# Kernel tuning notes

Measured on AMD Instinct MI355X. Metric: run time of the kernel, lower is better.

The kernel has to match this reference:

```python
import jax, jax.numpy as jnp
import numpy as np

B, N = 8, 2048
ZD, SD, MLP, DEPTH = 512, 64, 2048, 4


def setup_inputs() -> dict:
    key = jax.random.key(0)
    ks = jax.random.split(key, 8)
    g = lambda k, shape: jax.random.normal(k, shape, jnp.float32) * 0.02
    return {
        "z": jax.random.normal(ks[0], (B, N, ZD), jnp.float32),
        "spatial_embedding": jax.random.normal(ks[1], (B, N, SD), jnp.float32) * 0.5,
        "ln_z_scale": jnp.ones((DEPTH, ZD), jnp.float32),
        "ln_z_bias": jnp.zeros((DEPTH, ZD), jnp.float32),
        "ln_s_scale": jnp.ones((DEPTH, ZD), jnp.float32),
        "ln_s_bias": jnp.zeros((DEPTH, ZD), jnp.float32),
        "Wz1": g(ks[2], (DEPTH, ZD, MLP)), "bz1": jnp.zeros((DEPTH, MLP), jnp.float32),
        "Wz2": g(ks[3], (DEPTH, MLP, ZD)), "bz2": jnp.zeros((DEPTH, ZD), jnp.float32),
        "Ws1": g(ks[4], (DEPTH, ZD, MLP)), "bs1": jnp.zeros((DEPTH, MLP), jnp.float32),
        "Ws2": g(ks[5], (DEPTH, MLP, SD)), "bs2": jnp.zeros((DEPTH, SD), jnp.float32),
    }


def _layernorm(x, scale, bias, eps=1e-5):
    m = jnp.mean(x, axis=-1, keepdims=True)
    v = jnp.var(x, axis=-1, keepdims=True)  # biased var, matches torch LayerNorm
    return (x - m) * jax.lax.rsqrt(v + eps) * scale + bias


def _spatial_attn(e, z):
    # sim = exp(-||e_i - e_j||^2), row-normalized == softmax(-d2) over j.
    # Use |a|^2 + |b|^2 - 2ab expansion to avoid the [B,N,N,D] broadcast tensor.
    sq = jnp.sum(e * e, axis=-1)  # [B,N]
    d2 = sq[:, :, None] + sq[:, None, :] - 2.0 * jnp.einsum('bid,bjd->bij', e, e)
    d2 = jnp.maximum(d2, 0.0)
    attn = jax.nn.softmax(-d2, axis=-1)  # [B,N,N]
    return jnp.einsum('bij,bjd->bid', attn, z)


def _ff(x, W1, b1, W2, b2):
    h = jax.nn.gelu(x @ W1 + b1, approximate=False)  # torch nn.GELU() is exact erf
    return h @ W2 + b2


def reference(z, spatial_embedding, ln_z_scale, ln_z_bias, ln_s_scale, ln_s_bias,
              Wz1, bz1, Wz2, bz2, Ws1, bs1, Ws2, bs2):
    s = spatial_embedding
    for i in range(DEPTH):
        z = _spatial_attn(s, z)
        z = _ff(_layernorm(z, ln_z_scale[i], ln_z_bias[i]), Wz1[i], bz1[i], Wz2[i], bz2[i]) + z
        s = _ff(_layernorm(z, ln_s_scale[i], ln_s_bias[i]), Ws1[i], bs1[i], Ws2[i], bs2[i]) + s
    return (z, s)
```

## Files before the change

kernel.cpp:

```cpp
#include <hip/hip_runtime.h>
#include <stdint.h>

#define DEPTH 4
#define BATCH 8
#define NN 2048
#define ZDIM 512
#define SDIM 64
#define MLPD 2048
#define ROWS (BATCH*NN)

typedef __bf16 bf16x8_t __attribute__((ext_vector_type(8)));
typedef float f32x4_t __attribute__((ext_vector_type(4)));
typedef unsigned short us;

#define AS1 __attribute__((address_space(1)))
#define AS3 __attribute__((address_space(3)))

__device__ __forceinline__ void gload16(const void* g, void* l) {
  __builtin_amdgcn_global_load_lds((const AS1 void*)g, (AS3 void*)l, 16, 0, 0);
}

__device__ __forceinline__ unsigned short f2bf(float f) {
  union { float f; unsigned u; } v; v.f = f;
  unsigned u = v.u;
  unsigned r = (u + 0x7fffu + ((u >> 16) & 1u)) >> 16;
  return (unsigned short)r;
}
__device__ __forceinline__ float bf2f(unsigned short h) {
  union { unsigned u; float f; } v; v.u = ((unsigned)h) << 16;
  return v.f;
}

__device__ __forceinline__ float gelu_fast(float x) {
  float ax = fabsf(x) * 0.70710678118654752440f;
  float t = __builtin_amdgcn_rcpf(1.0f + 0.3275911f * ax);
  float p = t * (0.254829592f + t * (-0.284496736f + t * (1.421413741f +
            t * (-1.453152027f + t * 1.061405429f))));
  float er = 1.0f - p * __expf(-ax * ax);
  float s = (x >= 0.f) ? er : -er;
  return 0.5f * x * (1.0f + s);
}

#define LGKM0() do { asm volatile("s_waitcnt lgkmcnt(0)" ::: "memory"); \
                     __builtin_amdgcn_sched_barrier(0); } while (0)

__global__ __launch_bounds__(256) void conv_e_kernel(const float* __restrict__ s,
    unsigned short* __restrict__ ebf, float* __restrict__ sq) {
  int lane = threadIdx.x & 63;
  int row = blockIdx.x * 4 + (threadIdx.x >> 6);
  float x = s[(long)row * SDIM + lane];
  unsigned short v = f2bf(x);
  ebf[(long)row * SDIM + lane] = v;
  float xb = bf2f(v);
  float ss = xb * xb;
  #pragma unroll
  for (int off = 32; off > 0; off >>= 1) ss += __shfl_xor(ss, off);
  if (lane == 0) sq[row] = ss;
}

__global__ __launch_bounds__(256) void tconv_kernel(const float* __restrict__ in,
    unsigned short* __restrict__ out, int R, int C, long sIn, long sOut) {
  __shared__ float tile[32][33];
  int b = blockIdx.z;
  int c0 = blockIdx.x * 32, r0 = blockIdx.y * 32;
  int tx = threadIdx.x, ty = threadIdx.y;
  const float* ib = in + (long)b * sIn;
  unsigned short* ob = out + (long)b * sOut;
  #pragma unroll
  for (int i = 0; i < 32; i += 8)
    tile[ty + i][tx] = ib[(long)(r0 + ty + i) * C + c0 + tx];
  __syncthreads();
  #pragma unroll
  for (int i = 0; i < 32; i += 8)
    ob[(long)(c0 + ty + i) * R + r0 + tx] = f2bf(tile[tx][ty + i]);
}

__global__ __launch_bounds__(256) void ln_kernel(const float* __restrict__ x,
    const float* __restrict__ scale, const float* __restrict__ bias,
    unsigned short* __restrict__ y) {
  int lane = threadIdx.x & 63;
  long row = (long)blockIdx.x * 4 + (threadIdx.x >> 6);
  const float* xr = x + row * ZDIM + lane * 8;
  float4 v0 = *(const float4*)xr;
  float4 v1 = *(const float4*)(xr + 4);
  float xv[8] = {v0.x, v0.y, v0.z, v0.w, v1.x, v1.y, v1.z, v1.w};
  float s1 = 0.f, s2 = 0.f;
  #pragma unroll
  for (int k = 0; k < 8; ++k) { s1 += xv[k]; s2 += xv[k] * xv[k]; }
  #pragma unroll
  for (int off = 32; off > 0; off >>= 1) {
    s1 += __shfl_xor(s1, off);
    s2 += __shfl_xor(s2, off);
  }
  float mean = s1 * (1.0f / ZDIM);
  float var = s2 * (1.0f / ZDIM) - mean * mean;
  float rstd = rsqrtf(var + 1e-5f);
  const float* sc = scale + lane * 8;
  const float* bi = bias + lane * 8;
  alignas(16) unsigned short o[8];
  #pragma unroll
  for (int k = 0; k < 8; ++k)
    o[k] = f2bf((xv[k] - mean) * rstd * sc[k] + bi[k]);
  *(uint4*)(y + row * ZDIM + lane * 8) = *(const uint4*)o;
}

__global__ __launch_bounds__(256) void attn_w_kernel(const unsigned short* __restrict__ ebf,
    const float* __restrict__ sq, unsigned short* __restrict__ wout,
    float* __restrict__ RS) {
  __shared__ unsigned short Ei[4096];
  __shared__ unsigned short Ej[8192];
  __shared__ unsigned short Wt[8192];
  int tid = threadIdx.x, lane = tid & 63, wid = tid >> 6;
  int lr = lane & 15, hi = lane >> 4;
  int q = blockIdx.y;
  int b = blockIdx.z;
  int i0 = blockIdx.x * 64;
  const unsigned short* eb = ebf + (long)b * NN * SDIM;

  int rl = tid >> 3;
  int scs = ((tid & 7) ^ (rl & 7)) * 8;
  int dstc = (tid & 192) * 8;

  #pragma unroll
  for (int it = 0; it < 2; ++it)
    gload16(eb + (long)(i0 + it * 32 + rl) * SDIM + scs, &Ei[it * 2048 + dstc]);
  #pragma unroll
  for (int it = 0; it < 4; ++it)
    gload16(eb + (long)(q * 512 + it * 32 + rl) * SDIM + scs, &Ej[it * 2048 + dstc]);
  __syncthreads();

  bf16x8_t afrag[2];
  int ka = lr & 7;
  #pragma unroll
  for (int s = 0; s < 2; ++s)
    afrag[s] = *(const bf16x8_t*)&Ei[(wid * 16 + lr) * 64 + (((s * 4 + hi) ^ ka) * 8)];
  int rloc = wid * 16 + (hi << 2);
  float sqi[4];
  #pragma unroll
  for (int r = 0; r < 4; ++r) sqi[r] = sq[b * NN + i0 + rloc + r];
  float rs[4] = {0.f, 0.f, 0.f, 0.f};
  us* stripe = &Wt[wid * 2048];

  for (int jj = 0; jj < 4; ++jj) {
    int j0 = q * 512 + jj * 128;
    if (jj > 0) {
      __syncthreads();
      #pragma unroll
      for (int it = 0; it < 4; ++it)
        gload16(eb + (long)(j0 + it * 32 + rl) * SDIM + scs, &Ej[it * 2048 + dstc]);
      __syncthreads();
    }
    #pragma unroll
    for (int n = 0; n < 8; ++n) {
      f32x4_t g = {0.f, 0.f, 0.f, 0.f};
      #pragma unroll
      for (int s = 0; s < 2; ++s) {
        int rb = n * 16 + lr;
        bf16x8_t bfr = *(const bf16x8_t*)&Ej[rb * 64 + (((s * 4 + hi) ^ (rb & 7)) * 8)];
        g = __builtin_amdgcn_mfma_f32_16x16x32_bf16(afrag[s], bfr, g, 0, 0, 0);
      }
      float sqj = sq[b * NN + j0 + n * 16 + lr];
      #pragma unroll
      for (int r = 0; r < 4; ++r) {
        float d2 = sqi[r] + sqj - 2.0f * g[r];
        d2 = fmaxf(d2, 0.0f);
        float w = __expf(-d2);
        unsigned short wb = f2bf(w);
        rs[r] += bf2f(wb);
        int srow = (hi << 2) + r;
        stripe[srow * 128 + ((n ^ (srow & 3)) * 16) + lr] = wb;
      }
    }
    LGKM0();
    #pragma unroll
    for (int it = 0; it < 4; ++it) {
      int seg = it * 64 + lane;
      int row = seg >> 4, c8 = seg & 15;
      int c8s = c8 ^ ((row & 3) << 1);
      uint4 v = *(const uint4*)&stripe[row * 128 + c8s * 8];
      long gi = i0 + wid * 16 + row;
      *(uint4*)&wout[(long)b * NN * NN + gi * NN + j0 + c8 * 8] = v;
    }
  }
  #pragma unroll
  for (int off = 1; off < 16; off <<= 1) {
    #pragma unroll
    for (int r = 0; r < 4; ++r) rs[r] += __shfl_xor(rs[r], off);
  }
  if (lr == 0) {
    #pragma unroll
    for (int r = 0; r < 4; ++r)
      RS[(long)q * ROWS + b * NN + i0 + rloc + r] = rs[r];
  }
}

template <int EPI>
__global__ __launch_bounds__(256, 4) void gemm3b(
    const unsigned short* __restrict__ A, const unsigned short* __restrict__ BT,
    void* __restrict__ Cout, const float* __restrict__ bias,
    const float* __restrict__ resid, const float* __restrict__ RS,
    int Nmat, int K, long sA, long sB, long sC, long sR) {
  __shared__ unsigned short As[64 * 64];
  __shared__ unsigned short Bs[128 * 64];
  int tid = threadIdx.x, lane = tid & 63;
  int lr = lane & 15, hi = lane >> 4;
  int wid = tid >> 6, wr = wid >> 1, wc = wid & 1;
  int bb = blockIdx.z;

  int gx = gridDim.x;
  int wg = blockIdx.y * gx + blockIdx.x;
  int nwg = gx * gridDim.y;
  if ((nwg & 7) == 0) wg = (wg & 7) * (nwg >> 3) + (wg >> 3);
  int bj = wg % gx, bi = wg / gx;
  int row0 = bi * 64, col0 = bj * 128;

  const unsigned short* Ab = A + (long)bb * sA;
  const unsigned short* Bb = BT + (long)bb * sB;

  int rl = tid >> 3;
  int scs = ((tid & 7) ^ (rl & 7)) * 8;
  const unsigned short* pA[2];
  const unsigned short* pB[4];
  #pragma unroll
  for (int it = 0; it < 2; ++it)
    pA[it] = Ab + (long)(row0 + it * 32 + rl) * K + scs;
  #pragma unroll
  for (int it = 0; it < 4; ++it) {
    int rb = col0 + it * 32 + rl;
    if (rb > Nmat - 1) rb = Nmat - 1;
    pB[it] = Bb + (long)rb * K + scs;
  }
  int dstc = (tid & 192) * 8;

  int offA[2][2], offB[4][2];
  #pragma unroll
  for (int m = 0; m < 2; ++m)
    #pragma unroll
    for (int s = 0; s < 2; ++s) {
      int ra = wr * 32 + m * 16 + lr;
      offA[m][s] = ra * 64 + (((s * 4 + hi) ^ (ra & 7)) * 8);
    }
  #pragma unroll
  for (int n = 0; n < 4; ++n)
    #pragma unroll
    for (int s = 0; s < 2; ++s) {
      int rb = wc * 64 + n * 16 + lr;
      offB[n][s] = rb * 64 + (((s * 4 + hi) ^ (rb & 7)) * 8);
    }

  auto stage = [&]() {
    #pragma unroll
    for (int it = 0; it < 2; ++it) { gload16(pA[it], &As[it * 2048 + dstc]); pA[it] += 64; }
    #pragma unroll
    for (int it = 0; it < 4; ++it) { gload16(pB[it], &Bs[it * 2048 + dstc]); pB[it] += 64; }
  };

  const f32x4_t fzero = {0.f, 0.f, 0.f, 0.f};
  f32x4_t acc[2][4];
  #pragma unroll
  for (int m = 0; m < 2; ++m)
    #pragma unroll
    for (int n = 0; n < 4; ++n) acc[m][n] = fzero;

  int nk = K >> 6;
  stage();

  for (int t = 0; t < nk; ++t) {
    __syncthreads();
    bf16x8_t a0s0 = *(const bf16x8_t*)&As[offA[0][0]];
    bf16x8_t a1s0 = *(const bf16x8_t*)&As[offA[1][0]];
    bf16x8_t a0s1 = *(const bf16x8_t*)&As[offA[0][1]];
    bf16x8_t a1s1 = *(const bf16x8_t*)&As[offA[1][1]];
    bf16x8_t b0s0 = *(const bf16x8_t*)&Bs[offB[0][0]];
    bf16x8_t b1s0 = *(const bf16x8_t*)&Bs[offB[1][0]];
    bf16x8_t b2s0 = *(const bf16x8_t*)&Bs[offB[2][0]];
    bf16x8_t b3s0 = *(const bf16x8_t*)&Bs[offB[3][0]];
    bf16x8_t b0s1 = *(const bf16x8_t*)&Bs[offB[0][1]];
    bf16x8_t b1s1 = *(const bf16x8_t*)&Bs[offB[1][1]];
    bf16x8_t b2s1 = *(const bf16x8_t*)&Bs[offB[2][1]];
    bf16x8_t b3s1 = *(const bf16x8_t*)&Bs[offB[3][1]];
    __syncthreads();
    if (t + 1 < nk) stage();
    acc[0][0] = __builtin_amdgcn_mfma_f32_16x16x32_bf16(a0s0, b0s0, acc[0][0], 0, 0, 0);
    acc[1][0] = __builtin_amdgcn_mfma_f32_16x16x32_bf16(a1s0, b0s0, acc[1][0], 0, 0, 0);
    acc[0][1] = __builtin_amdgcn_mfma_f32_16x16x32_bf16(a0s0, b1s0, acc[0][1], 0, 0, 0);
    acc[1][1] = __builtin_amdgcn_mfma_f32_16x16x32_bf16(a1s0, b1s0, acc[1][1], 0, 0, 0);
    acc[0][2] = __builtin_amdgcn_mfma_f32_16x16x32_bf16(a0s0, b2s0, acc[0][2], 0, 0, 0);
    acc[1][2] = __builtin_amdgcn_mfma_f32_16x16x32_bf16(a1s0, b2s0, acc[1][2], 0, 0, 0);
    acc[0][3] = __builtin_amdgcn_mfma_f32_16x16x32_bf16(a0s0, b3s0, acc[0][3], 0, 0, 0);
    acc[1][3] = __builtin_amdgcn_mfma_f32_16x16x32_bf16(a1s0, b3s0, acc[1][3], 0, 0, 0);
    acc[0][0] = __builtin_amdgcn_mfma_f32_16x16x32_bf16(a0s1, b0s1, acc[0][0], 0, 0, 0);
    acc[1][0] = __builtin_amdgcn_mfma_f32_16x16x32_bf16(a1s1, b0s1, acc[1][0], 0, 0, 0);
    acc[0][1] = __builtin_amdgcn_mfma_f32_16x16x32_bf16(a0s1, b1s1, acc[0][1], 0, 0, 0);
    acc[1][1] = __builtin_amdgcn_mfma_f32_16x16x32_bf16(a1s1, b1s1, acc[1][1], 0, 0, 0);
    acc[0][2] = __builtin_amdgcn_mfma_f32_16x16x32_bf16(a0s1, b2s1, acc[0][2], 0, 0, 0);
    acc[1][2] = __builtin_amdgcn_mfma_f32_16x16x32_bf16(a1s1, b2s1, acc[1][2], 0, 0, 0);
    acc[0][3] = __builtin_amdgcn_mfma_f32_16x16x32_bf16(a0s1, b3s1, acc[0][3], 0, 0, 0);
    acc[1][3] = __builtin_amdgcn_mfma_f32_16x16x32_bf16(a1s1, b3s1, acc[1][3], 0, 0, 0);
  }

  int rbase = row0 + wr * 32 + hi * 4;
  int cbase = col0 + wc * 64 + lr;
  if (EPI == 1) {
    float bv[4];
    #pragma unroll
    for (int n = 0; n < 4; ++n) bv[n] = bias[cbase + n * 16];
    us* stripe = &Bs[wid * 2048];
    #pragma unroll
    for (int m = 0; m < 2; ++m) {
      #pragma unroll
      for (int r = 0; r < 4; ++r) {
        int sr = m * 16 + hi * 4 + r;
        #pragma unroll
        for (int n = 0; n < 4; ++n)
          stripe[sr * 64 + ((n ^ (sr & 3)) * 16) + lr] =
              f2bf(gelu_fast(acc[m][n][r] + bv[n]));
      }
    }
    LGKM0();
    unsigned short* Cb = (unsigned short*)Cout;
    #pragma unroll
    for (int it = 0; it < 4; ++it) {
      int seg = it * 64 + lane;
      int sr = seg >> 3, c8 = seg & 7;
      int c8s = c8 ^ ((sr & 3) << 1);
      uint4 v = *(const uint4*)&stripe[sr * 64 + c8s * 8];
      long row = row0 + wr * 32 + sr;
      *(uint4*)&Cb[row * Nmat + col0 + wc * 64 + c8 * 8] = v;
    }
  } else {
    #pragma unroll
    for (int m = 0; m < 2; ++m) {
      #pragma unroll
      for (int r = 0; r < 4; ++r) {
        int row = rbase + m * 16 + r;
        float ir = 0.f;
        if (EPI == 0) {
          long idx = (long)bb * sR + row;
          float den = RS[idx] + RS[ROWS + idx] + RS[2L * ROWS + idx] + RS[3L * ROWS + idx];
          ir = 1.0f / den;
        }
        #pragma unroll
        for (int n = 0; n < 4; ++n) {
          int col = cbase + n * 16;
          if (col >= Nmat) continue;
          float v = acc[m][n][r];
          long cidx = (long)bb * sC + (long)row * Nmat + col;
          if (EPI == 0) {
            ((float*)Cout)[cidx] = v * ir;
          } else {
            ((float*)Cout)[cidx] = v + bias[col] + resid[(long)bb * sR + (long)row * Nmat + col];
          }
        }
      }
    }
  }
}

extern "C" void kernel_launch(void* const* d_in, const int* in_sizes, int n_in,
                              void* d_out, int out_size, void* d_ws, size_t ws_size,
                              hipStream_t stream) {
  (void)in_sizes; (void)n_in; (void)out_size; (void)ws_size;
  const float* in_z   = (const float*)d_in[0];
  const float* in_s   = (const float*)d_in[1];
  const float* lnz_sc = (const float*)d_in[2];
  const float* lnz_bi = (const float*)d_in[3];
  const float* lns_sc = (const float*)d_in[4];
  const float* lns_bi = (const float*)d_in[5];
  const float* Wz1 = (const float*)d_in[6];
  const float* bz1 = (const float*)d_in[7];
  const float* Wz2 = (const float*)d_in[8];
  const float* bz2 = (const float*)d_in[9];
  const float* Ws1 = (const float*)d_in[10];
  const float* bs1 = (const float*)d_in[11];
  const float* Ws2 = (const float*)d_in[12];
  const float* bs2 = (const float*)d_in[13];
  float* out_z = (float*)d_out;
  float* out_s = out_z + (long)ROWS * ZDIM;

  char* ws = (char*)d_ws;
  size_t off = 0;
  auto alloc = [&](size_t bytes) { void* p = ws + off; off += (bytes + 255) & ~(size_t)255; return p; };
  unsigned short* WH   = (unsigned short*)alloc((size_t)BATCH * NN * NN * 2);
  unsigned short* ZT   = (unsigned short*)alloc((size_t)BATCH * ZDIM * NN * 2);
  unsigned short* XLN  = (unsigned short*)alloc((size_t)ROWS * ZDIM * 2);
  unsigned short* EBF  = (unsigned short*)alloc((size_t)ROWS * SDIM * 2);
  float* ZATT = (float*)alloc((size_t)ROWS * ZDIM * 4);
  float* ZBUF = (float*)alloc((size_t)ROWS * ZDIM * 4);
  float* SBUF = (float*)alloc((size_t)ROWS * SDIM * 4);
  float* SQ   = (float*)alloc((size_t)ROWS * 4);
  float* RS   = (float*)alloc((size_t)4 * ROWS * 4);
  unsigned short* W1Z = (unsigned short*)alloc((size_t)DEPTH * MLPD * ZDIM * 2);
  unsigned short* W2Z = (unsigned short*)alloc((size_t)DEPTH * ZDIM * MLPD * 2);
  unsigned short* W1S = (unsigned short*)alloc((size_t)DEPTH * MLPD * ZDIM * 2);
  unsigned short* W2S = (unsigned short*)alloc((size_t)DEPTH * SDIM * MLPD * 2);

  tconv_kernel<<<dim3(MLPD / 32, ZDIM / 32, DEPTH), dim3(32, 8), 0, stream>>>(
      Wz1, W1Z, ZDIM, MLPD, (long)ZDIM * MLPD, (long)MLPD * ZDIM);
  tconv_kernel<<<dim3(ZDIM / 32, MLPD / 32, DEPTH), dim3(32, 8), 0, stream>>>(
      Wz2, W2Z, MLPD, ZDIM, (long)MLPD * ZDIM, (long)ZDIM * MLPD);
  tconv_kernel<<<dim3(MLPD / 32, ZDIM / 32, DEPTH), dim3(32, 8), 0, stream>>>(
      Ws1, W1S, ZDIM, MLPD, (long)ZDIM * MLPD, (long)MLPD * ZDIM);
  tconv_kernel<<<dim3(SDIM / 32, MLPD / 32, DEPTH), dim3(32, 8), 0, stream>>>(
      Ws2, W2S, MLPD, SDIM, (long)MLPD * SDIM, (long)SDIM * MLPD);

  for (int L = 0; L < DEPTH; ++L) {
    const float* z_in = (L == 0) ? in_z : ZBUF;
    const float* s_in = (L == 0) ? in_s : SBUF;
    float* z_out = (L == DEPTH - 1) ? out_z : ZBUF;
    float* s_out = (L == DEPTH - 1) ? out_s : SBUF;

    conv_e_kernel<<<ROWS / 4, 256, 0, stream>>>(s_in, EBF, SQ);
    tconv_kernel<<<dim3(ZDIM / 32, NN / 32, BATCH), dim3(32, 8), 0, stream>>>(
        z_in, ZT, NN, ZDIM, (long)NN * ZDIM, (long)ZDIM * NN);
    attn_w_kernel<<<dim3(NN / 64, 4, BATCH), 256, 0, stream>>>(EBF, SQ, WH, RS);
    gemm3b<0><<<dim3(ZDIM / 128, NN / 64, BATCH), 256, 0, stream>>>(
        WH, ZT, ZATT, nullptr, nullptr, RS,
        ZDIM, NN, (long)NN * NN, (long)ZDIM * NN, (long)NN * ZDIM, NN);
    ln_kernel<<<ROWS / 4, 256, 0, stream>>>(ZATT, lnz_sc + L * ZDIM, lnz_bi + L * ZDIM, XLN);
    gemm3b<1><<<dim3(MLPD / 128, ROWS / 64, 1), 256, 0, stream>>>(
        XLN, W1Z + (long)L * MLPD * ZDIM, WH, bz1 + L * MLPD, nullptr, nullptr,
        MLPD, ZDIM, 0, 0, 0, 0);
    gemm3b<2><<<dim3(ZDIM / 128, ROWS / 64, 1), 256, 0, stream>>>(
        WH, W2Z + (long)L * ZDIM * MLPD, z_out, bz2 + L * ZDIM, ZATT, nullptr,
        ZDIM, MLPD, 0, 0, 0, 0);
    ln_kernel<<<ROWS / 4, 256, 0, stream>>>(z_out, lns_sc + L * ZDIM, lns_bi + L * ZDIM, XLN);
    gemm3b<1><<<dim3(MLPD / 128, ROWS / 64, 1), 256, 0, stream>>>(
        XLN, W1S + (long)L * MLPD * ZDIM, WH, bs1 + L * MLPD, nullptr, nullptr,
        MLPD, ZDIM, 0, 0, 0, 0);
    gemm3b<2><<<dim3(1, ROWS / 64, 1), 256, 0, stream>>>(
        WH, W2S + (long)L * SDIM * MLPD, s_out, bs2 + L * SDIM, s_in, nullptr,
        SDIM, MLPD, 0, 0, 0, 0);
  }
}
```

Measured before the change: 1.125 ms.

## Fuse attention weight computation with PV GEMM in a flash-style kernel

```diff
diff --git a/kernel.cpp b/kernel.cpp
--- a/kernel.cpp
+++ b/kernel.cpp
@@ -43,6 +43,7 @@
 
 #define LGKM0() do { asm volatile("s_waitcnt lgkmcnt(0)" ::: "memory"); \
                      __builtin_amdgcn_sched_barrier(0); } while (0)
+#define MF(A_, B_, C_) __builtin_amdgcn_mfma_f32_16x16x32_bf16(A_, B_, C_, 0, 0, 0)
 
 __global__ __launch_bounds__(256) void conv_e_kernel(const float* __restrict__ s,
     unsigned short* __restrict__ ebf, float* __restrict__ sq) {
@@ -104,93 +105,143 @@
   *(uint4*)(y + row * ZDIM + lane * 8) = *(const uint4*)o;
 }
 
-__global__ __launch_bounds__(256) void attn_w_kernel(const unsigned short* __restrict__ ebf,
-    const float* __restrict__ sq, unsigned short* __restrict__ wout,
-    float* __restrict__ RS) {
-  __shared__ unsigned short Ei[4096];
-  __shared__ unsigned short Ej[8192];
-  __shared__ unsigned short Wt[8192];
+__global__ __launch_bounds__(256, 2) void attn_pv_kernel(
+    const unsigned short* __restrict__ ebf, const float* __restrict__ sq,
+    const unsigned short* __restrict__ ZTg, float* __restrict__ Oout) {
+  __shared__ unsigned short Ei[2048];
+  __shared__ unsigned short Ej[2][8192];
+  __shared__ unsigned short Pl[2][4096];
+  __shared__ float RSs[4][32];
   int tid = threadIdx.x, lane = tid & 63, wid = tid >> 6;
   int lr = lane & 15, hi = lane >> 4;
-  int q = blockIdx.y;
   int b = blockIdx.z;
-  int i0 = blockIdx.x * 64;
+  int i0 = blockIdx.x * 32;
   const unsigned short* eb = ebf + (long)b * NN * SDIM;
+  const unsigned short* zb = ZTg + (long)b * ZDIM * NN;
 
   int rl = tid >> 3;
   int scs = ((tid & 7) ^ (rl & 7)) * 8;
   int dstc = (tid & 192) * 8;
 
-  #pragma unroll
-  for (int it = 0; it < 2; ++it)
-    gload16(eb + (long)(i0 + it * 32 + rl) * SDIM + scs, &Ei[it * 2048 + dstc]);
+  gload16(eb + (long)(i0 + rl) * SDIM + scs, &Ei[dstc]);
   #pragma unroll
   for (int it = 0; it < 4; ++it)
-    gload16(eb + (long)(q * 512 + it * 32 + rl) * SDIM + scs, &Ej[it * 2048 + dstc]);
+    gload16(eb + (long)(it * 32 + rl) * SDIM + scs, &Ej[0][it * 2048 + dstc]);
+
+  float sqi[2][4];
+  #pragma unroll
+  for (int m = 0; m < 2; ++m)
+    #pragma unroll
+    for (int r = 0; r < 4; ++r)
+      sqi[m][r] = sq[b * NN + i0 + m * 16 + hi * 4 + r];
+
+  const unsigned short* bp[8];
+  #pragma unroll
+  for (int n = 0; n < 8; ++n)
+    bp[n] = zb + (long)(wid * 128 + n * 16 + lr) * NN + hi * 8;
+
+  f32x4_t acc[2][8];
+  #pragma unroll
+  for (int m = 0; m < 2; ++m)
+    #pragma unroll
+    for (int n = 0; n < 8; ++n) acc[m][n] = (f32x4_t){0.f, 0.f, 0.f, 0.f};
+  float rsum[2][4] = {{0.f, 0.f, 0.f, 0.f}, {0.f, 0.f, 0.f, 0.f}};
+
   __syncthreads();
 
-  bf16x8_t afrag[2];
   int ka = lr & 7;
-  #pragma unroll
-  for (int s = 0; s < 2; ++s)
-    afrag[s] = *(const bf16x8_t*)&Ei[(wid * 16 + lr) * 64 + (((s * 4 + hi) ^ ka) * 8)];
-  int rloc = wid * 16 + (hi << 2);
-  float sqi[4];
-  #pragma unroll
-  for (int r = 0; r < 4; ++r) sqi[r] = sq[b * NN + i0 + rloc + r];
-  float rs[4] = {0.f, 0.f, 0.f, 0.f};
-  us* stripe = &Wt[wid * 2048];
-
-  for (int jj = 0; jj < 4; ++jj) {
-    int j0 = q * 512 + jj * 128;
-    if (jj > 0) {
-      __syncthreads();
+  for (int jt = 0; jt < NN / 128; ++jt) {
+    int buf = jt & 1;
+    int j0 = jt * 128;
+
+    f32x4_t sacc[2][2];
+    #pragma unroll
+    for (int m = 0; m < 2; ++m)
+      #pragma unroll
+      for (int n = 0; n < 2; ++n) sacc[m][n] = (f32x4_t){0.f, 0.f, 0.f, 0.f};
+    #pragma unroll
+    for (int k2 = 0; k2 < 2; ++k2) {
+      int kc = ((k2 * 4 + hi) ^ ka) * 8;
+      bf16x8_t af0 = *(const bf16x8_t*)&Ei[lr * 64 + kc];
+      bf16x8_t af1 = *(const bf16x8_t*)&Ei[(16 + lr) * 64 + kc];
+      bf16x8_t bf0 = *(const bf16x8_t*)&Ej[buf][(wid * 32 + lr) * 64 + kc];
+      bf16x8_t bf1 = *(const bf16x8_t*)&Ej[buf][(wid * 32 + 16 + lr) * 64 + kc];
+      sacc[0][0] = MF(af0, bf0, sacc[0][0]);
+      sacc[1][0] = MF(af1, bf0, sacc[1][0]);
+      sacc[0][1] = MF(af0, bf1, sacc[0][1]);
+      sacc[1][1] = MF(af1, bf1, sacc[1][1]);
+    }
+    float sqj0 = sq[b * NN + j0 + wid * 32 + lr];
+    float sqj1 = sq[b * NN + j0 + wid * 32 + 16 + lr];
+    #pragma unroll
+    for (int m = 0; m < 2; ++m) {
+      #pragma unroll
+      for (int n = 0; n < 2; ++n) {
+        float sqjn = n ? sqj1 : sqj0;
+        #pragma unroll
+        for (int r = 0; r < 4; ++r) {
+          int row = m * 16 + hi * 4 + r;
+          float d2 = fmaxf(sqi[m][r] + sqjn - 2.0f * sacc[m][n][r], 0.0f);
+          unsigned short wb = f2bf(__expf(-d2));
+          rsum[m][r] += bf2f(wb);
+          int c8 = wid * 4 + n * 2 + (lr >> 3);
+          Pl[buf][row * 128 + ((c8 ^ (row & 7)) * 8) + (lr & 7)] = wb;
+        }
+      }
+    }
+    __syncthreads();
+
+    if (jt + 1 < NN / 128) {
       #pragma unroll
       for (int it = 0; it < 4; ++it)
-        gload16(eb + (long)(j0 + it * 32 + rl) * SDIM + scs, &Ej[it * 2048 + dstc]);
-      __syncthreads();
-    }
-    #pragma unroll
-    for (int n = 0; n < 8; ++n) {
-      f32x4_t g = {0.f, 0.f, 0.f, 0.f};
-      #pragma unroll
-      for (int s = 0; s < 2; ++s) {
-        int rb = n * 16 + lr;
-        bf16x8_t bfr = *(const bf16x8_t*)&Ej[rb * 64 + (((s * 4 + hi) ^ (rb & 7)) * 8)];
-        g = __builtin_amdgcn_mfma_f32_16x16x32_bf16(afrag[s], bfr, g, 0, 0, 0);
+        gload16(eb + (long)((jt + 1) * 128 + it * 32 + rl) * SDIM + scs,
+                &Ej[buf ^ 1][it * 2048 + dstc]);
+    }
+
+    bf16x8_t bv[2][8];
+    #pragma unroll
+    for (int n = 0; n < 8; ++n) bv[0][n] = *(const bf16x8_t*)(bp[n] + j0);
+    #pragma unroll
+    for (int kf = 0; kf < 4; ++kf) {
+      int cb = kf & 1;
+      if (kf < 3) {
+        #pragma unroll
+        for (int n = 0; n < 8; ++n)
+          bv[cb ^ 1][n] = *(const bf16x8_t*)(bp[n] + j0 + (kf + 1) * 32);
       }
-      float sqj = sq[b * NN + j0 + n * 16 + lr];
-      #pragma unroll
-      for (int r = 0; r < 4; ++r) {
-        float d2 = sqi[r] + sqj - 2.0f * g[r];
-        d2 = fmaxf(d2, 0.0f);
-        float w = __expf(-d2);
-        unsigned short wb = f2bf(w);
-        rs[r] += bf2f(wb);
-        int srow = (hi << 2) + r;
-        stripe[srow * 128 + ((n ^ (srow & 3)) * 16) + lr] = wb;
+      int pc = ((kf * 4 + hi) ^ ka) * 8;
+      bf16x8_t pa0 = *(const bf16x8_t*)&Pl[buf][lr * 128 + pc];
+      bf16x8_t pa1 = *(const bf16x8_t*)&Pl[buf][(16 + lr) * 128 + pc];
+      #pragma unroll
+      for (int n = 0; n < 8; ++n) {
+        acc[0][n] = MF(pa0, bv[cb][n], acc[0][n]);
+        acc[1][n] = MF(pa1, bv[cb][n], acc[1][n]);
       }
     }
-    LGKM0();
-    #pragma unroll
-    for (int it = 0; it < 4; ++it) {
-      int seg = it * 64 + lane;
-      int row = seg >> 4, c8 = seg & 15;
-      int c8s = c8 ^ ((row & 3) << 1);
-      uint4 v = *(const uint4*)&stripe[row * 128 + c8s * 8];
-      long gi = i0 + wid * 16 + row;
-      *(uint4*)&wout[(long)b * NN * NN + gi * NN + j0 + c8 * 8] = v;
-    }
-  }
-  #pragma unroll
-  for (int off = 1; off < 16; off <<= 1) {
-    #pragma unroll
-    for (int r = 0; r < 4; ++r) rs[r] += __shfl_xor(rs[r], off);
-  }
-  if (lr == 0) {
-    #pragma unroll
-    for (int r = 0; r < 4; ++r)
-      RS[(long)q * ROWS + b * NN + i0 + rloc + r] = rs[r];
+    __syncthreads();
+  }
+
+  #pragma unroll
+  for (int m = 0; m < 2; ++m)
+    #pragma unroll
+    for (int r = 0; r < 4; ++r) {
+      float v = rsum[m][r];
+      v += __shfl_xor(v, 1); v += __shfl_xor(v, 2);
+      v += __shfl_xor(v, 4); v += __shfl_xor(v, 8);
+      if (lr == 0) RSs[wid][m * 16 + hi * 4 + r] = v;
+    }
+  __syncthreads();
+  float* ob = Oout + ((long)b * NN + i0) * ZDIM + wid * 128;
+  #pragma unroll
+  for (int m = 0; m < 2; ++m) {
+    #pragma unroll
+    for (int r = 0; r < 4; ++r) {
+      int row = m * 16 + hi * 4 + r;
+      float inv = 1.0f / (RSs[0][row] + RSs[1][row] + RSs[2][row] + RSs[3][row]);
+      #pragma unroll
+      for (int n = 0; n < 8; ++n)
+        ob[(long)row * ZDIM + n * 16 + lr] = acc[m][n][r] * inv;
+    }
   }
 }
 
@@ -198,14 +249,13 @@
 __global__ __launch_bounds__(256, 4) void gemm3b(
     const unsigned short* __restrict__ A, const unsigned short* __restrict__ BT,
     void* __restrict__ Cout, const float* __restrict__ bias,
-    const float* __restrict__ resid, const float* __restrict__ RS,
-    int Nmat, int K, long sA, long sB, long sC, long sR) {
+    const float* __restrict__ resid,
+    int Nmat, int K, long sC, long sR) {
   __shared__ unsigned short As[64 * 64];
   __shared__ unsigned short Bs[128 * 64];
   int tid = threadIdx.x, lane = tid & 63;
   int lr = lane & 15, hi = lane >> 4;
   int wid = tid >> 6, wr = wid >> 1, wc = wid & 1;
-  int bb = blockIdx.z;
 
   int gx = gridDim.x;
   int wg = blockIdx.y * gx + blockIdx.x;
@@ -214,21 +264,18 @@
   int bj = wg % gx, bi = wg / gx;
   int row0 = bi * 64, col0 = bj * 128;
 
-  const unsigned short* Ab = A + (long)bb * sA;
-  const unsigned short* Bb = BT + (long)bb * sB;
-
   int rl = tid >> 3;
   int scs = ((tid & 7) ^ (rl & 7)) * 8;
   const unsigned short* pA[2];
   const unsigned short* pB[4];
   #pragma unroll
   for (int it = 0; it < 2; ++it)
-    pA[it] = Ab + (long)(row0 + it * 32 + rl) * K + scs;
+    pA[it] = A + (long)(row0 + it * 32 + rl) * K + scs;
   #pragma unroll
   for (int it = 0; it < 4; ++it) {
     int rb = col0 + it * 32 + rl;
     if (rb > Nmat - 1) rb = Nmat - 1;
-    pB[it] = Bb + (long)rb * K + scs;
+    pB[it] = BT + (long)rb * K + scs;
   }
   int dstc = (tid & 192) * 8;
 
@@ -255,12 +302,11 @@
     for (int it = 0; it < 4; ++it) { gload16(pB[it], &Bs[it * 2048 + dstc]); pB[it] += 64; }
   };
 
-  const f32x4_t fzero = {0.f, 0.f, 0.f, 0.f};
   f32x4_t acc[2][4];
   #pragma unroll
   for (int m = 0; m < 2; ++m)
     #pragma unroll
-    for (int n = 0; n < 4; ++n) acc[m][n] = fzero;
+    for (int n = 0; n < 4; ++n) acc[m][n] = (f32x4_t){0.f, 0.f, 0.f, 0.f};
 
   int nk = K >> 6;
   stage();
@@ -281,22 +327,22 @@
     bf16x8_t b3s1 = *(const bf16x8_t*)&Bs[offB[3][1]];
     __syncthreads();
     if (t + 1 < nk) stage();
-    acc[0][0] = __builtin_amdgcn_mfma_f32_16x16x32_bf16(a0s0, b0s0, acc[0][0], 0, 0, 0);
-    acc[1][0] = __builtin_amdgcn_mfma_f32_16x16x32_bf16(a1s0, b0s0, acc[1][0], 0, 0, 0);
-    acc[0][1] = __builtin_amdgcn_mfma_f32_16x16x32_bf16(a0s0, b1s0, acc[0][1], 0, 0, 0);
-    acc[1][1] = __builtin_amdgcn_mfma_f32_16x16x32_bf16(a1s0, b1s0, acc[1][1], 0, 0, 0);
-    acc[0][2] = __builtin_amdgcn_mfma_f32_16x16x32_bf16(a0s0, b2s0, acc[0][2], 0, 0, 0);
-    acc[1][2] = __builtin_amdgcn_mfma_f32_16x16x32_bf16(a1s0, b2s0, acc[1][2], 0, 0, 0);
-    acc[0][3] = __builtin_amdgcn_mfma_f32_16x16x32_bf16(a0s0, b3s0, acc[0][3], 0, 0, 0);
-    acc[1][3] = __builtin_amdgcn_mfma_f32_16x16x32_bf16(a1s0, b3s0, acc[1][3], 0, 0, 0);
-    acc[0][0] = __builtin_amdgcn_mfma_f32_16x16x32_bf16(a0s1, b0s1, acc[0][0], 0, 0, 0);
-    acc[1][0] = __builtin_amdgcn_mfma_f32_16x16x32_bf16(a1s1, b0s1, acc[1][0], 0, 0, 0);
-    acc[0][1] = __builtin_amdgcn_mfma_f32_16x16x32_bf16(a0s1, b1s1, acc[0][1], 0, 0, 0);
-    acc[1][1] = __builtin_amdgcn_mfma_f32_16x16x32_bf16(a1s1, b1s1, acc[1][1], 0, 0, 0);
-    acc[0][2] = __builtin_amdgcn_mfma_f32_16x16x32_bf16(a0s1, b2s1, acc[0][2], 0, 0, 0);
-    acc[1][2] = __builtin_amdgcn_mfma_f32_16x16x32_bf16(a1s1, b2s1, acc[1][2], 0, 0, 0);
-    acc[0][3] = __builtin_amdgcn_mfma_f32_16x16x32_bf16(a0s1, b3s1, acc[0][3], 0, 0, 0);
-    acc[1][3] = __builtin_amdgcn_mfma_f32_16x16x32_bf16(a1s1, b3s1, acc[1][3], 0, 0, 0);
+    acc[0][0] = MF(a0s0, b0s0, acc[0][0]);
+    acc[1][0] = MF(a1s0, b0s0, acc[1][0]);
+    acc[0][1] = MF(a0s0, b1s0, acc[0][1]);
+    acc[1][1] = MF(a1s0, b1s0, acc[1][1]);
+    acc[0][2] = MF(a0s0, b2s0, acc[0][2]);
+    acc[1][2] = MF(a1s0, b2s0, acc[1][2]);
+    acc[0][3] = MF(a0s0, b3s0, acc[0][3]);
+    acc[1][3] = MF(a1s0, b3s0, acc[1][3]);
+    acc[0][0] = MF(a0s1, b0s1, acc[0][0]);
+    acc[1][0] = MF(a1s1, b0s1, acc[1][0]);
+    acc[0][1] = MF(a0s1, b1s1, acc[0][1]);
+    acc[1][1] = MF(a1s1, b1s1, acc[1][1]);
+    acc[0][2] = MF(a0s1, b2s1, acc[0][2]);
+    acc[1][2] = MF(a1s1, b2s1, acc[1][2]);
+    acc[0][3] = MF(a0s1, b3s1, acc[0][3]);
+    acc[1][3] = MF(a1s1, b3s1, acc[1][3]);
   }
 
   int rbase = row0 + wr * 32 + hi * 4;
@@ -334,23 +380,13 @@
       #pragma unroll
       for (int r = 0; r < 4; ++r) {
         int row = rbase + m * 16 + r;
-        float ir = 0.f;
-        if (EPI == 0) {
-          long idx = (long)bb * sR + row;
-          float den = RS[idx] + RS[ROWS + idx] + RS[2L * ROWS + idx] + RS[3L * ROWS + idx];
-          ir = 1.0f / den;
-        }
         #pragma unroll
         for (int n = 0; n < 4; ++n) {
           int col = cbase + n * 16;
           if (col >= Nmat) continue;
           float v = acc[m][n][r];
-          long cidx = (long)bb * sC + (long)row * Nmat + col;
-          if (EPI == 0) {
-            ((float*)Cout)[cidx] = v * ir;
-          } else {
-            ((float*)Cout)[cidx] = v + bias[col] + resid[(long)bb * sR + (long)row * Nmat + col];
-          }
+          ((float*)Cout)[(long)row * sC + col] =
+              v + bias[col] + resid[(long)row * sR + col];
         }
       }
     }
@@ -381,7 +417,7 @@
   char* ws = (char*)d_ws;
   size_t off = 0;
   auto alloc = [&](size_t bytes) { void* p = ws + off; off += (bytes + 255) & ~(size_t)255; return p; };
-  unsigned short* WH   = (unsigned short*)alloc((size_t)BATCH * NN * NN * 2);
+  unsigned short* WH   = (unsigned short*)alloc((size_t)ROWS * MLPD * 2);
   unsigned short* ZT   = (unsigned short*)alloc((size_t)BATCH * ZDIM * NN * 2);
   unsigned short* XLN  = (unsigned short*)alloc((size_t)ROWS * ZDIM * 2);
   unsigned short* EBF  = (unsigned short*)alloc((size_t)ROWS * SDIM * 2);
@@ -389,7 +425,6 @@
   float* ZBUF = (float*)alloc((size_t)ROWS * ZDIM * 4);
   float* SBUF = (float*)alloc((size_t)ROWS * SDIM * 4);
   float* SQ   = (float*)alloc((size_t)ROWS * 4);
-  float* RS   = (float*)alloc((size_t)4 * ROWS * 4);
   unsigned short* W1Z = (unsigned short*)alloc((size_t)DEPTH * MLPD * ZDIM * 2);
   unsigned short* W2Z = (unsigned short*)alloc((size_t)DEPTH * ZDIM * MLPD * 2);
   unsigned short* W1S = (unsigned short*)alloc((size_t)DEPTH * MLPD * ZDIM * 2);
@@ -413,23 +448,20 @@
     conv_e_kernel<<<ROWS / 4, 256, 0, stream>>>(s_in, EBF, SQ);
     tconv_kernel<<<dim3(ZDIM / 32, NN / 32, BATCH), dim3(32, 8), 0, stream>>>(
         z_in, ZT, NN, ZDIM, (long)NN * ZDIM, (long)ZDIM * NN);
-    attn_w_kernel<<<dim3(NN / 64, 4, BATCH), 256, 0, stream>>>(EBF, SQ, WH, RS);
-    gemm3b<0><<<dim3(ZDIM / 128, NN / 64, BATCH), 256, 0, stream>>>(
-        WH, ZT, ZATT, nullptr, nullptr, RS,
-        ZDIM, NN, (long)NN * NN, (long)ZDIM * NN, (long)NN * ZDIM, NN);
+    attn_pv_kernel<<<dim3(NN / 32, 1, BATCH), 256, 0, stream>>>(EBF, SQ, ZT, ZATT);
     ln_kernel<<<ROWS / 4, 256, 0, stream>>>(ZATT, lnz_sc + L * ZDIM, lnz_bi + L * ZDIM, XLN);
     gemm3b<1><<<dim3(MLPD / 128, ROWS / 64, 1), 256, 0, stream>>>(
-        XLN, W1Z + (long)L * MLPD * ZDIM, WH, bz1 + L * MLPD, nullptr, nullptr,
-        MLPD, ZDIM, 0, 0, 0, 0);
+        XLN, W1Z + (long)L * MLPD * ZDIM, WH, bz1 + L * MLPD, nullptr,
+        MLPD, ZDIM, 0, 0);
     gemm3b<2><<<dim3(ZDIM / 128, ROWS / 64, 1), 256, 0, stream>>>(
-        WH, W2Z + (long)L * ZDIM * MLPD, z_out, bz2 + L * ZDIM, ZATT, nullptr,
-        ZDIM, MLPD, 0, 0, 0, 0);
+        WH, W2Z + (long)L * ZDIM * MLPD, z_out, bz2 + L * ZDIM, ZATT,
+        ZDIM, MLPD, ZDIM, ZDIM);
     ln_kernel<<<ROWS / 4, 256, 0, stream>>>(z_out, lns_sc + L * ZDIM, lns_bi + L * ZDIM, XLN);
     gemm3b<1><<<dim3(MLPD / 128, ROWS / 64, 1), 256, 0, stream>>>(
-        XLN, W1S + (long)L * MLPD * ZDIM, WH, bs1 + L * MLPD, nullptr, nullptr,
-        MLPD, ZDIM, 0, 0, 0, 0);
+        XLN, W1S + (long)L * MLPD * ZDIM, WH, bs1 + L * MLPD, nullptr,
+        MLPD, ZDIM, 0, 0);
     gemm3b<2><<<dim3(1, ROWS / 64, 1), 256, 0, stream>>>(
-        WH, W2S + (long)L * SDIM * MLPD, s_out, bs2 + L * SDIM, s_in, nullptr,
-        SDIM, MLPD, 0, 0, 0, 0);
-  }
-}
+        WH, W2S + (long)L * SDIM * MLPD, s_out, bs2 + L * SDIM, s_in,
+        SDIM, MLPD, SDIM, SDIM);
+  }
+}
```

Result: slower. 1.388 ms (+23.4%).
